# Performance work log

Hardware: AMD Instinct MI355X
Metric: run time of the kernel (lower is better)

## Reference

```python
import jax, jax.numpy as jnp
import numpy as np

B, T, D, HS = 8, 2048, 768, 64  # batch, seq, n_embd, head_size


def setup_inputs() -> dict:
    key = jax.random.key(0)
    kx, kq, kk, kv = jax.random.split(key, 4)
    scale = 1.0 / np.sqrt(D)
    return {
        "x": jax.random.normal(kx, (B, T, D), dtype=jnp.float32),
        "Wq": jax.random.normal(kq, (D, HS), dtype=jnp.float32) * scale,
        "Wk": jax.random.normal(kk, (D, HS), dtype=jnp.float32) * scale,
        "Wv": jax.random.normal(kv, (D, HS), dtype=jnp.float32) * scale,
    }


def reference(x, Wq, Wk, Wv):
    # q,k,v: [B,T,HS]
    q = jnp.einsum("btd,dh->bth", x, Wq)
    k = jnp.einsum("btd,dh->bth", x, Wk)
    v = jnp.einsum("btd,dh->bth", x, Wv)
    hs = k.shape[-1]
    # scaled scores: [B,T,T]
    wei = jnp.einsum("bth,bsh->bts", q, k) * (hs ** -0.5)
    # causal mask (lower-triangular keeps, upper -> -inf)
    causal = jnp.tril(jnp.ones((x.shape[1], x.shape[1]), dtype=bool))
    wei = jnp.where(causal[None, :, :], wei, -jnp.inf)
    wei = jax.nn.softmax(wei, axis=-1)
    return jnp.einsum("bts,bsh->bth", wei, v)
```

## Files before the change

### kernel.cpp

```cpp
#include <hip/hip_runtime.h>

typedef float  f32x4  __attribute__((ext_vector_type(4)));
typedef short  short8 __attribute__((ext_vector_type(8)));
typedef short  short4_ __attribute__((ext_vector_type(4)));

constexpr int Bb = 8, T = 2048, D = 768, HS = 64;
constexpr int BT = Bb * T;
constexpr int QT = T / 64;
constexpr int PSTRIDE = 64 * 64 + 128;

__device__ __forceinline__ short f2bf(float f) {
    unsigned u = __builtin_bit_cast(unsigned, f);
    unsigned r = (u + 0x7FFFu + ((u >> 16) & 1u)) >> 16;
    return (short)r;
}

__device__ __forceinline__ void gld_lds16(const short* g, short* l) {
    __builtin_amdgcn_global_load_lds(
        (const __attribute__((address_space(1))) unsigned int*)g,
        (__attribute__((address_space(3))) unsigned int*)l, 16, 0, 0);
}

__global__ __launch_bounds__(256) void wt_kernel(const float* __restrict__ Wq,
                                                 const float* __restrict__ Wk,
                                                 const float* __restrict__ Wv,
                                                 short* __restrict__ Wt) {
    int n = blockIdx.x;
    const float* W = (n < 64) ? Wq : (n < 128) ? Wk : Wv;
    int c = n & 63;
    for (int kk = threadIdx.x; kk < D; kk += 256)
        Wt[n * D + kk] = f2bf(W[kk * HS + c]);
}

__global__ __launch_bounds__(512) void qkv_proj(const float* __restrict__ x,
                                                const short* __restrict__ Wt,
                                                short* __restrict__ qws,
                                                short* __restrict__ kws,
                                                short* __restrict__ vtg) {
    __shared__ alignas(16) short xs[2][32 * 72];
    __shared__ alignas(16) short wtile[2][192 * 64];

    const int tid  = threadIdx.x;
    const int lane = tid & 63, w = tid >> 6;
    const int lo   = lane & 15, hi = lane >> 4;
    const int wr   = w >> 2, wc = w & 3;
    const int row0 = blockIdx.x * 32;
    const int b    = row0 >> 11, t0 = row0 & 2047;

    const int sxr = tid >> 4, sxs = tid & 15;
    const float* xsrc = &x[(size_t)(row0 + sxr) * D + sxs * 4];

    f32x4 acc[3];
#pragma unroll
    for (int j = 0; j < 3; j++) acc[j] = f32x4{0.f, 0.f, 0.f, 0.f};

#define STAGE(bb, kc)                                                         \
    {                                                                         \
        _Pragma("unroll")                                                     \
        for (int it = 0; it < 3; it++) {                                      \
            int ci = it * 512 + w * 64 + lane;                                \
            int n = ci >> 3, seg = ci & 7;                                    \
            gld_lds16(&Wt[(size_t)n * D + (kc) * 64 + seg * 8],               \
                      &wtile[bb][(it * 512 + w * 64) * 8]);                   \
        }                                                                     \
        float4 f = *reinterpret_cast<const float4*>(xsrc + (kc) * 64);        \
        short4_ h;                                                            \
        h[0] = f2bf(f.x); h[1] = f2bf(f.y); h[2] = f2bf(f.z); h[3] = f2bf(f.w);\
        *reinterpret_cast<short4_*>(&xs[bb][sxr * 72 + sxs * 4]) = h;         \
    }

    STAGE(0, 0);
    __syncthreads();

    for (int kc = 0; kc < 12; kc++) {
        const int bb = kc & 1;
        if (kc + 1 < 12) STAGE(bb ^ 1, kc + 1);

        const int arow = (wr * 16 + lo) * 72;
        short8 a0 = *reinterpret_cast<const short8*>(&xs[bb][arow + hi * 8]);
        short8 a1 = *reinterpret_cast<const short8*>(&xs[bb][arow + 32 + hi * 8]);
#pragma unroll
        for (int j = 0; j < 3; j++) {
            const int c = (wc * 48 + j * 16 + lo) * 64;
            short8 b0 = *reinterpret_cast<const short8*>(&wtile[bb][c + hi * 8]);
            short8 b1 = *reinterpret_cast<const short8*>(&wtile[bb][c + 32 + hi * 8]);
            acc[j] = __builtin_amdgcn_mfma_f32_16x16x32_bf16(a0, b0, acc[j], 0, 0, 0);
            acc[j] = __builtin_amdgcn_mfma_f32_16x16x32_bf16(a1, b1, acc[j], 0, 0, 0);
        }
        __syncthreads();
    }
#undef STAGE

    const int orow = row0 + wr * 16 + hi * 4;
#pragma unroll
    for (int j = 0; j < 3; j++) {
        const int cb = wc * 48 + j * 16;
        if (cb < 64) {
#pragma unroll
            for (int r = 0; r < 4; r++)
                qws[(size_t)(orow + r) * HS + cb + lo] = f2bf(acc[j][r] * 0.125f);
        } else if (cb < 128) {
#pragma unroll
            for (int r = 0; r < 4; r++)
                kws[(size_t)(orow + r) * HS + cb - 64 + lo] = f2bf(acc[j][r]);
        } else {
            short4_ pv;
#pragma unroll
            for (int r = 0; r < 4; r++) pv[r] = f2bf(acc[j][r]);
            *reinterpret_cast<short4_*>(
                &vtg[((size_t)b * 64 + cb - 128 + lo) * T + t0 + wr * 16 + hi * 4]) = pv;
        }
    }
}

__global__ __launch_bounds__(256) void attn(const short* __restrict__ qg,
                                            const short* __restrict__ kg,
                                            const short* __restrict__ vtg,
                                            float* __restrict__ part, int S) {
    __shared__ short ks[2][64 * 64];
    __shared__ short vts[2][64 * 64];
    __shared__ short ps[4][16 * 64];

    const int tid  = threadIdx.x;
    const int lane = tid & 63, w = tid >> 6;
    const int lo   = lane & 15, hi = lane >> 4;
    const int bid  = blockIdx.x;
    const int per_b = QT * S;
    const int b    = bid / per_b;
    const int r2   = bid % per_b;
    const int qt   = 31 - (r2 / S);
    const int c    = r2 % S;
    const int nkt  = qt + 1;
    const int base = nkt / S, rem = nkt % S;
    const int niter = base + (c < rem ? 1 : 0);
    const int kt0   = c * base + (c < rem ? c : rem);
    float* pout = part + (size_t)((b * QT + qt) * S + c) * PSTRIDE;

    float m_[4], l_[4];
    f32x4 oacc[4];
#pragma unroll
    for (int r = 0; r < 4; r++) { m_[r] = -1e30f; l_[r] = 0.0f; }
#pragma unroll
    for (int i = 0; i < 4; i++) oacc[i] = f32x4{0.f, 0.f, 0.f, 0.f};

    if (niter > 0) {
        const int qrow = qt * 64 + w * 16 + lo;
        const size_t qbase = ((size_t)b * T + qrow) * HS;
        short8 qa0 = *reinterpret_cast<const short8*>(&qg[qbase + hi * 8]);
        short8 qa1 = *reinterpret_cast<const short8*>(&qg[qbase + 32 + hi * 8]);

        const int srow = tid >> 2, scs = tid & 3, r7 = srow & 7;
        const int w0 = srow * 64 + (((scs * 2)     ^ r7) << 3);
        const int w1 = srow * 64 + (((scs * 2 + 1) ^ r7) << 3);
        const size_t kgoff = (size_t)b * T * HS;
        const size_t vgoff = ((size_t)b * 64 + srow) * T;

        short8 ka, kb2, va, vb;
        {
            const short* kp = &kg[kgoff + (size_t)(kt0 * 64 + srow) * HS + scs * 16];
            ka = *reinterpret_cast<const short8*>(kp);
            kb2 = *reinterpret_cast<const short8*>(kp + 8);
            const short* vp = &vtg[vgoff + kt0 * 64 + scs * 16];
            va = *reinterpret_cast<const short8*>(vp);
            vb = *reinterpret_cast<const short8*>(vp + 8);
        }
        *reinterpret_cast<short8*>(&ks[0][w0])  = ka;
        *reinterpret_cast<short8*>(&ks[0][w1])  = kb2;
        *reinterpret_cast<short8*>(&vts[0][w0]) = va;
        *reinterpret_cast<short8*>(&vts[0][w1]) = vb;

        int cur = 0;
        for (int i = 0; i < niter; i++) {
            const int kt = kt0 + i;
            if (i + 1 < niter) {
                const short* kp = &kg[kgoff + (size_t)((kt + 1) * 64 + srow) * HS + scs * 16];
                ka = *reinterpret_cast<const short8*>(kp);
                kb2 = *reinterpret_cast<const short8*>(kp + 8);
                const short* vp = &vtg[vgoff + (kt + 1) * 64 + scs * 16];
                va = *reinterpret_cast<const short8*>(vp);
                vb = *reinterpret_cast<const short8*>(vp + 8);
            }
            __syncthreads();

            f32x4 sacc[4];
#pragma unroll
            for (int nt = 0; nt < 4; nt++) sacc[nt] = f32x4{0.f, 0.f, 0.f, 0.f};
            __builtin_amdgcn_s_setprio(1);
#pragma unroll
            for (int nt = 0; nt < 4; nt++) {
                const int row = nt * 16 + lo, rr = row & 7;
                short8 b0 = *reinterpret_cast<const short8*>(
                    &ks[cur][row * 64 + ((hi ^ rr) << 3)]);
                short8 b1 = *reinterpret_cast<const short8*>(
                    &ks[cur][row * 64 + (((hi + 4) ^ rr) << 3)]);
                sacc[nt] = __builtin_amdgcn_mfma_f32_16x16x32_bf16(qa0, b0, sacc[nt], 0, 0, 0);
                sacc[nt] = __builtin_amdgcn_mfma_f32_16x16x32_bf16(qa1, b1, sacc[nt], 0, 0, 0);
            }
            __builtin_amdgcn_s_setprio(0);

            if (kt == qt) {
#pragma unroll
                for (int nt = 0; nt < 4; nt++)
#pragma unroll
                    for (int r = 0; r < 4; r++)
                        if (nt * 16 + lo > w * 16 + hi * 4 + r) sacc[nt][r] = -1e30f;
            }

#pragma unroll
            for (int r = 0; r < 4; r++) {
                float t0m = fmaxf(fmaxf(sacc[0][r], sacc[1][r]),
                                  fmaxf(sacc[2][r], sacc[3][r]));
#pragma unroll
                for (int off = 1; off < 16; off <<= 1) t0m = fmaxf(t0m, __shfl_xor(t0m, off));
                float mnew = fmaxf(m_[r], t0m);
                float corr = __expf(m_[r] - mnew);
                float psum = 0.0f;
#pragma unroll
                for (int nt = 0; nt < 4; nt++) {
                    float p = __expf(sacc[nt][r] - mnew);
                    sacc[nt][r] = p;
                    psum += p;
                }
#pragma unroll
                for (int off = 1; off < 16; off <<= 1) psum += __shfl_xor(psum, off);
                l_[r] = l_[r] * corr + psum;
                m_[r] = mnew;
#pragma unroll
                for (int nt = 0; nt < 4; nt++) oacc[nt][r] *= corr;
            }

#pragma unroll
            for (int nt = 0; nt < 4; nt++)
#pragma unroll
                for (int r = 0; r < 4; r++) {
                    const int qr = hi * 4 + r;
                    const int seg = nt * 2 + (lo >> 3);
                    ps[w][qr * 64 + ((seg ^ (qr & 7)) << 3) + (lo & 7)] = f2bf(sacc[nt][r]);
                }

            const int pl7 = lo & 7;
            short8 pa0 = *reinterpret_cast<const short8*>(
                &ps[w][lo * 64 + ((hi ^ pl7) << 3)]);
            short8 pa1 = *reinterpret_cast<const short8*>(
                &ps[w][lo * 64 + (((hi + 4) ^ pl7) << 3)]);
            __builtin_amdgcn_s_setprio(1);
#pragma unroll
            for (int nt = 0; nt < 4; nt++) {
                const int row = nt * 16 + lo, rr = row & 7;
                short8 b0 = *reinterpret_cast<const short8*>(
                    &vts[cur][row * 64 + ((hi ^ rr) << 3)]);
                short8 b1 = *reinterpret_cast<const short8*>(
                    &vts[cur][row * 64 + (((hi + 4) ^ rr) << 3)]);
                oacc[nt] = __builtin_amdgcn_mfma_f32_16x16x32_bf16(pa0, b0, oacc[nt], 0, 0, 0);
                oacc[nt] = __builtin_amdgcn_mfma_f32_16x16x32_bf16(pa1, b1, oacc[nt], 0, 0, 0);
            }
            __builtin_amdgcn_s_setprio(0);

            if (i + 1 < niter) {
                *reinterpret_cast<short8*>(&ks[cur ^ 1][w0])  = ka;
                *reinterpret_cast<short8*>(&ks[cur ^ 1][w1])  = kb2;
                *reinterpret_cast<short8*>(&vts[cur ^ 1][w0]) = va;
                *reinterpret_cast<short8*>(&vts[cur ^ 1][w1]) = vb;
            }
            cur ^= 1;
        }
    }

#pragma unroll
    for (int nt = 0; nt < 4; nt++)
#pragma unroll
        for (int r = 0; r < 4; r++)
            pout[(w * 16 + hi * 4 + r) * 64 + nt * 16 + lo] = oacc[nt][r];
    if (lo == 0) {
#pragma unroll
        for (int r = 0; r < 4; r++) {
            const int row = w * 16 + hi * 4 + r;
            pout[4096 + row] = m_[r];
            pout[4160 + row] = l_[r];
        }
    }
}

__global__ __launch_bounds__(256) void combine(const float* __restrict__ part,
                                               float* __restrict__ out, int S) {
    const int bid = blockIdx.x;
    const int b = bid >> 5, qt = bid & 31;
    const float* p = part + (size_t)bid * S * PSTRIDE;
    const int row = threadIdx.x >> 2, cs = threadIdx.x & 3;

    float mv[4], lv[4], av[4];
    float M = -1e30f;
    for (int s = 0; s < S; s++) {
        mv[s] = p[(size_t)s * PSTRIDE + 4096 + row];
        lv[s] = p[(size_t)s * PSTRIDE + 4160 + row];
        M = fmaxf(M, mv[s]);
    }
    float den = 0.0f;
    for (int s = 0; s < S; s++) { av[s] = __expf(mv[s] - M); den += lv[s] * av[s]; }
    float inv = 1.0f / den;

    float* o = out + ((size_t)b * T + qt * 64 + row) * HS + cs * 16;
#pragma unroll
    for (int i = 0; i < 4; i++) {
        float4 res = make_float4(0.f, 0.f, 0.f, 0.f);
        for (int s = 0; s < S; s++) {
            float4 v = *reinterpret_cast<const float4*>(
                p + (size_t)s * PSTRIDE + row * 64 + cs * 16 + i * 4);
            res.x += v.x * av[s]; res.y += v.y * av[s];
            res.z += v.z * av[s]; res.w += v.w * av[s];
        }
        res.x *= inv; res.y *= inv; res.z *= inv; res.w *= inv;
        *reinterpret_cast<float4*>(o + i * 4) = res;
    }
}

extern "C" void kernel_launch(void* const* d_in, const int* in_sizes, int n_in,
                              void* d_out, int out_size, void* d_ws, size_t ws_size,
                              hipStream_t stream) {
    const float* x  = (const float*)d_in[0];
    const float* Wq = (const float*)d_in[1];
    const float* Wk = (const float*)d_in[2];
    const float* Wv = (const float*)d_in[3];
    float* out = (float*)d_out;

    short* ws   = (short*)d_ws;
    short* qws  = ws;
    short* kws  = qws + (size_t)BT * HS;
    short* vtws = kws + (size_t)BT * HS;
    short* Wt   = vtws + (size_t)BT * HS;
    float* part = (float*)(Wt + (size_t)192 * D);

    const size_t fixed = (size_t)3 * BT * HS * 2 + (size_t)192 * D * 2;
    int S = 4;
    while (S > 1 && fixed + (size_t)Bb * QT * S * PSTRIDE * 4 > ws_size) S >>= 1;

    wt_kernel<<<192, 256, 0, stream>>>(Wq, Wk, Wv, Wt);
    qkv_proj<<<BT / 32, 512, 0, stream>>>(x, Wt, qws, kws, vtws);
    attn<<<Bb * QT * S, 256, 0, stream>>>(qws, kws, vtws, part, S);
    combine<<<Bb * QT, 256, 0, stream>>>(part, out, S);
}
```

Before: 64.31 us.

## Double QKV projection row tile and XOR-swizzle weight tile in LDS

The QKV projection block now handles 64 rows instead of 32. Each wave computes two 16-row M subtiles, so every weight tile staged in LDS is reused across twice as many rows and only half as many blocks are launched. The weight tile is stored with an XOR swizzle on its 16-byte segments, keyed by row, to cut LDS bank conflicts on the B-operand reads. The cost is twice as many accumulators, a larger x buffer in LDS, and fewer blocks (256) to fill the GPU.

```diff
diff --git a/kernel.cpp b/kernel.cpp
--- a/kernel.cpp
+++ b/kernel.cpp
@@ -37,36 +37,40 @@
                                                 short* __restrict__ qws,
                                                 short* __restrict__ kws,
                                                 short* __restrict__ vtg) {
-    __shared__ alignas(16) short xs[2][32 * 72];
+    __shared__ alignas(16) short xs[2][64 * 72];
     __shared__ alignas(16) short wtile[2][192 * 64];
 
     const int tid  = threadIdx.x;
     const int lane = tid & 63, w = tid >> 6;
     const int lo   = lane & 15, hi = lane >> 4;
     const int wr   = w >> 2, wc = w & 3;
-    const int row0 = blockIdx.x * 32;
+    const int row0 = blockIdx.x * 64;
     const int b    = row0 >> 11, t0 = row0 & 2047;
 
-    const int sxr = tid >> 4, sxs = tid & 15;
-    const float* xsrc = &x[(size_t)(row0 + sxr) * D + sxs * 4];
-
-    f32x4 acc[3];
-#pragma unroll
-    for (int j = 0; j < 3; j++) acc[j] = f32x4{0.f, 0.f, 0.f, 0.f};
-
-#define STAGE(bb, kc)                                                         \
-    {                                                                         \
-        _Pragma("unroll")                                                     \
-        for (int it = 0; it < 3; it++) {                                      \
-            int ci = it * 512 + w * 64 + lane;                                \
-            int n = ci >> 3, seg = ci & 7;                                    \
-            gld_lds16(&Wt[(size_t)n * D + (kc) * 64 + seg * 8],               \
-                      &wtile[bb][(it * 512 + w * 64) * 8]);                   \
-        }                                                                     \
-        float4 f = *reinterpret_cast<const float4*>(xsrc + (kc) * 64);        \
-        short4_ h;                                                            \
-        h[0] = f2bf(f.x); h[1] = f2bf(f.y); h[2] = f2bf(f.z); h[3] = f2bf(f.w);\
-        *reinterpret_cast<short4_*>(&xs[bb][sxr * 72 + sxs * 4]) = h;         \
+    const int xr0 = tid >> 4, xsg = tid & 15;
+    const float* xsrc0 = &x[(size_t)(row0 + xr0) * D + xsg * 4];
+    const float* xsrc1 = &x[(size_t)(row0 + 32 + xr0) * D + xsg * 4];
+
+    f32x4 acc[6];
+#pragma unroll
+    for (int j = 0; j < 6; j++) acc[j] = f32x4{0.f, 0.f, 0.f, 0.f};
+
+#define STAGE(bb, kc)                                                          \
+    {                                                                          \
+        _Pragma("unroll")                                                      \
+        for (int it = 0; it < 3; it++) {                                       \
+            int ci = it * 512 + w * 64 + lane;                                 \
+            int n = ci >> 3, seg = ci & 7;                                     \
+            gld_lds16(&Wt[(size_t)n * D + (kc) * 64 + ((seg ^ (n & 7)) << 3)], \
+                      &wtile[bb][(it * 512 + w * 64) * 8]);                    \
+        }                                                                      \
+        float4 f0 = *reinterpret_cast<const float4*>(xsrc0 + (kc) * 64);       \
+        float4 f1 = *reinterpret_cast<const float4*>(xsrc1 + (kc) * 64);       \
+        short4_ h0, h1;                                                        \
+        h0[0] = f2bf(f0.x); h0[1] = f2bf(f0.y); h0[2] = f2bf(f0.z); h0[3] = f2bf(f0.w); \
+        h1[0] = f2bf(f1.x); h1[1] = f2bf(f1.y); h1[2] = f2bf(f1.z); h1[3] = f2bf(f1.w); \
+        *reinterpret_cast<short4_*>(&xs[bb][xr0 * 72 + xsg * 4]) = h0;         \
+        *reinterpret_cast<short4_*>(&xs[bb][(32 + xr0) * 72 + xsg * 4]) = h1;  \
     }
 
     STAGE(0, 0);
@@ -76,39 +80,49 @@
         const int bb = kc & 1;
         if (kc + 1 < 12) STAGE(bb ^ 1, kc + 1);
 
-        const int arow = (wr * 16 + lo) * 72;
-        short8 a0 = *reinterpret_cast<const short8*>(&xs[bb][arow + hi * 8]);
-        short8 a1 = *reinterpret_cast<const short8*>(&xs[bb][arow + 32 + hi * 8]);
+#pragma unroll
+        for (int m = 0; m < 2; m++) {
+            const int ar = (wr * 32 + m * 16 + lo) * 72;
+            short8 a0 = *reinterpret_cast<const short8*>(&xs[bb][ar + hi * 8]);
+            short8 a1 = *reinterpret_cast<const short8*>(&xs[bb][ar + 32 + hi * 8]);
+#pragma unroll
+            for (int j = 0; j < 3; j++) {
+                const int row = wc * 48 + j * 16 + lo;
+                const int rx  = (row & 7) << 3;
+                short8 b0 = *reinterpret_cast<const short8*>(
+                    &wtile[bb][row * 64 + ((hi << 3) ^ rx)]);
+                short8 b1 = *reinterpret_cast<const short8*>(
+                    &wtile[bb][row * 64 + (((hi + 4) << 3) ^ rx)]);
+                acc[m * 3 + j] = __builtin_amdgcn_mfma_f32_16x16x32_bf16(a0, b0, acc[m * 3 + j], 0, 0, 0);
+                acc[m * 3 + j] = __builtin_amdgcn_mfma_f32_16x16x32_bf16(a1, b1, acc[m * 3 + j], 0, 0, 0);
+            }
+        }
+        __syncthreads();
+    }
+#undef STAGE
+
+#pragma unroll
+    for (int m = 0; m < 2; m++) {
+        const int orow = row0 + wr * 32 + m * 16 + hi * 4;
 #pragma unroll
         for (int j = 0; j < 3; j++) {
-            const int c = (wc * 48 + j * 16 + lo) * 64;
-            short8 b0 = *reinterpret_cast<const short8*>(&wtile[bb][c + hi * 8]);
-            short8 b1 = *reinterpret_cast<const short8*>(&wtile[bb][c + 32 + hi * 8]);
-            acc[j] = __builtin_amdgcn_mfma_f32_16x16x32_bf16(a0, b0, acc[j], 0, 0, 0);
-            acc[j] = __builtin_amdgcn_mfma_f32_16x16x32_bf16(a1, b1, acc[j], 0, 0, 0);
-        }
-        __syncthreads();
-    }
-#undef STAGE
-
-    const int orow = row0 + wr * 16 + hi * 4;
-#pragma unroll
-    for (int j = 0; j < 3; j++) {
-        const int cb = wc * 48 + j * 16;
-        if (cb < 64) {
-#pragma unroll
-            for (int r = 0; r < 4; r++)
-                qws[(size_t)(orow + r) * HS + cb + lo] = f2bf(acc[j][r] * 0.125f);
-        } else if (cb < 128) {
-#pragma unroll
-            for (int r = 0; r < 4; r++)
-                kws[(size_t)(orow + r) * HS + cb - 64 + lo] = f2bf(acc[j][r]);
-        } else {
-            short4_ pv;
-#pragma unroll
-            for (int r = 0; r < 4; r++) pv[r] = f2bf(acc[j][r]);
-            *reinterpret_cast<short4_*>(
-                &vtg[((size_t)b * 64 + cb - 128 + lo) * T + t0 + wr * 16 + hi * 4]) = pv;
+            const int cb = wc * 48 + j * 16;
+            const f32x4 a = acc[m * 3 + j];
+            if (cb < 64) {
+#pragma unroll
+                for (int r = 0; r < 4; r++)
+                    qws[(size_t)(orow + r) * HS + cb + lo] = f2bf(a[r] * 0.125f);
+            } else if (cb < 128) {
+#pragma unroll
+                for (int r = 0; r < 4; r++)
+                    kws[(size_t)(orow + r) * HS + cb - 64 + lo] = f2bf(a[r]);
+            } else {
+                short4_ pv;
+#pragma unroll
+                for (int r = 0; r < 4; r++) pv[r] = f2bf(a[r]);
+                *reinterpret_cast<short4_*>(
+                    &vtg[((size_t)b * 64 + cb - 128 + lo) * T + t0 + wr * 32 + m * 16 + hi * 4]) = pv;
+            }
         }
     }
 }
@@ -335,7 +349,7 @@
     while (S > 1 && fixed + (size_t)Bb * QT * S * PSTRIDE * 4 > ws_size) S >>= 1;
 
     wt_kernel<<<192, 256, 0, stream>>>(Wq, Wk, Wv, Wt);
-    qkv_proj<<<BT / 32, 512, 0, stream>>>(x, Wt, qws, kws, vtws);
+    qkv_proj<<<BT / 64, 512, 0, stream>>>(x, Wt, qws, kws, vtws);
     attn<<<Bb * QT * S, 256, 0, stream>>>(qws, kws, vtws, part, S);
     combine<<<Bb * QT, 256, 0, stream>>>(part, out, S);
 }
```

New measurement: 63.42 us. Within noise of the previous version (-1.4%).
